# Optimization experiments

Measured on AMD Instinct MI355X. Metric: run time of the kernel, lower is better.

## Reference

```python
import jax, jax.numpy as jnp
import numpy as np

N_NODES = 10000
IN_FEATS = 50
HIDDEN = 512
OUT_FEATS = 121
N_EDGES = 160000


def setup_inputs() -> dict:
    key = jax.random.key(0)
    ks = jax.random.split(key, 8)
    x = jax.random.normal(ks[0], (N_NODES, IN_FEATS), dtype=jnp.float32)
    edge_index = jax.random.randint(ks[1], (2, N_EDGES), 0, N_NODES, dtype=jnp.int64)
    # SAGEConv params: lin_l applied to aggregated neighbors (carries bias), lin_r to self.
    def glorot(k, fan_in, fan_out):
        s = jnp.sqrt(6.0 / (fan_in + fan_out))
        return jax.random.uniform(k, (fan_in, fan_out), minval=-s, maxval=s, dtype=jnp.float32)
    W1_l = glorot(ks[2], IN_FEATS, HIDDEN)
    W1_r = glorot(ks[3], IN_FEATS, HIDDEN)
    b1 = jnp.zeros((HIDDEN,), dtype=jnp.float32)
    W2_l = glorot(ks[4], HIDDEN, OUT_FEATS)
    W2_r = glorot(ks[5], HIDDEN, OUT_FEATS)
    b2 = jnp.zeros((OUT_FEATS,), dtype=jnp.float32)
    return {"x": x, "edge_index": edge_index, "W1_l": W1_l, "W1_r": W1_r,
            "b1": b1, "W2_l": W2_l, "W2_r": W2_r, "b2": b2}


def _mean_agg(h, src, dst, n_nodes):
    # gather source features per edge, segment-sum at destination, divide by in-degree
    summed = jax.ops.segment_sum(h[src], dst, num_segments=n_nodes)  # [N, F]
    deg = jax.ops.segment_sum(jnp.ones((src.shape[0],), h.dtype), dst, num_segments=n_nodes)
    return summed / jnp.maximum(deg, 1.0)[:, None]


def _sage_conv(h, src, dst, W_l, W_r, b, n_nodes):
    agg = _mean_agg(h, src, dst, n_nodes)
    return agg @ W_l + h @ W_r + b


def reference(x, edge_index, W1_l, W1_r, b1, W2_l, W2_r, b2):
    src, dst = edge_index[0], edge_index[1]
    n = x.shape[0]
    h = _sage_conv(x, src, dst, W1_l, W1_r, b1, n)
    h = jax.nn.relu(h)
    # dropout is identity in eval mode
    out = _sage_conv(h, src, dst, W2_l, W2_r, b2, n)
    return out
```

## Files before the change

kernel.cpp:

```cpp
#include <hip/hip_runtime.h>
#include <hip/hip_bf16.h>

constexpr int NN   = 10000;
constexpr int INF  = 50;
constexpr int HID  = 512;
constexpr int OUTF = 121;
constexpr int NE   = 160000;
constexpr int DMAX = 64;

typedef __attribute__((ext_vector_type(8))) short short8;
typedef __attribute__((ext_vector_type(4))) float floatx4;

__device__ inline float bf2f(unsigned short u) {
    union { unsigned int i; float f; } v; v.i = ((unsigned)u) << 16; return v.f;
}
__device__ inline unsigned short f2bf(float f) {
    __hip_bfloat16 h = __float2bfloat16(f);
    return *(unsigned short*)&h;
}



__global__ __launch_bounds__(256) void k_fillprep(const int* __restrict__ srcv, const int* __restrict__ dstv,
                                                  unsigned* __restrict__ cursor, int* __restrict__ csr,
                                                  const float* __restrict__ x,
                                                  const float* __restrict__ W1l, const float* __restrict__ W1r,
                                                  const float* __restrict__ W2l, const float* __restrict__ W2r,
                                                  __hip_bfloat16* __restrict__ xp,
                                                  __hip_bfloat16* __restrict__ B1p, __hip_bfloat16* __restrict__ B2p) {
    int b = blockIdx.x;
    if (b < 625) {
        unsigned V = cursor[NN];
        int e = b * 256 + threadIdx.x;
        if (e < NE) {
            int d = dstv[e];
            if ((unsigned)d < (unsigned)NN) {
                int pos = (int)(atomicAdd(&cursor[d], 1u) - V);
                int s = min(max(srcv[e], 0), NN - 1);
                if ((unsigned)pos < (unsigned)DMAX) csr[d * DMAX + pos] = s;
            }
        }
    } else {
        int idx = (b - 625) * 256 + threadIdx.x;
        if (idx < 65536) {
            int j = idx & 7, L = (idx >> 3) & 63, kt = (idx >> 9) & 3, nt = idx >> 11;
            int k = kt * 32 + ((L >> 4) * 8 + j);
            int n = nt * 16 + (L & 15);
            float v = (k < 50) ? W1l[k * HID + n] : ((k < 100) ? W1r[(k - 50) * HID + n] : 0.f);
            B1p[idx] = __float2bfloat16(v);
        }
        {
            int j = idx & 7, L = (idx >> 3) & 63, kt = (idx >> 9) & 15, nt = idx >> 13;
            int k = kt * 32 + ((L >> 4) * 8 + j);
            int n = nt * 16 + (L & 15);
            float v;
            if (n < 128) v = (n < OUTF) ? W2l[k * OUTF + n] : 0.f;
            else { int c = n - 128; v = (c < OUTF) ? W2r[k * OUTF + c] : 0.f; }
            B2p[idx] = __float2bfloat16(v);
        }
        for (int r = idx; r < NN * 64; r += 131072) {
            int n = r >> 6, c = r & 63;
            xp[r] = __float2bfloat16(c < INF ? x[n * INF + c] : 0.f);
        }
    }
}


__global__ __launch_bounds__(1024, 4) void k_fused(const __hip_bfloat16* __restrict__ xp,
                                                   const unsigned* __restrict__ cursor, const int* __restrict__ csr,
                                                   const __hip_bfloat16* __restrict__ B1p,
                                                   const float* __restrict__ b1,
                                                   const __hip_bfloat16* __restrict__ B2p,
                                                   __hip_bfloat16* __restrict__ Pb,
                                                   __hip_bfloat16* __restrict__ Qb) {
    __shared__ __align__(16) unsigned short As[16 * 136];
    __shared__ __align__(16) unsigned short Ht[16 * 520];
    int t = threadIdx.x;
    int w = t >> 6, lane = t & 63, quad = lane >> 4, l16 = lane & 15;
    int m0 = blockIdx.x * 16;
    const unsigned short* xs = (const unsigned short*)xp;

    {
        int nu = __builtin_amdgcn_readfirstlane(m0 + w);
        unsigned V = cursor[NN];
        int dt = (int)(cursor[nu] - V);
        int d = min(dt, DMAX);
        const int* crow = csr + nu * DMAX;
        const unsigned* xw = (const unsigned*)xp;
        int half = lane >> 5;
        int cp = lane & 31;
        float lo0 = 0.f, hi0 = 0.f, lo1 = 0.f, hi1 = 0.f;
        float lo2 = 0.f, hi2 = 0.f, lo3 = 0.f, hi3 = 0.f;
        int j = 0;
        for (; j + 8 <= d; j += 8) {
            int a0 = crow[j],     b0 = crow[j + 1];
            int a1 = crow[j + 2], b1i = crow[j + 3];
            int a2 = crow[j + 4], b2i = crow[j + 5];
            int a3 = crow[j + 6], b3i = crow[j + 7];
            int r0 = half ? b0 : a0;
            int r1 = half ? b1i : a1;
            int r2 = half ? b2i : a2;
            int r3 = half ? b3i : a3;
            unsigned u0 = xw[r0 * 32 + cp];
            unsigned u1 = xw[r1 * 32 + cp];
            unsigned u2 = xw[r2 * 32 + cp];
            unsigned u3 = xw[r3 * 32 + cp];
            lo0 += __uint_as_float(u0 << 16); hi0 += __uint_as_float(u0 & 0xffff0000u);
            lo1 += __uint_as_float(u1 << 16); hi1 += __uint_as_float(u1 & 0xffff0000u);
            lo2 += __uint_as_float(u2 << 16); hi2 += __uint_as_float(u2 & 0xffff0000u);
            lo3 += __uint_as_float(u3 << 16); hi3 += __uint_as_float(u3 & 0xffff0000u);
        }
        for (; j + 2 <= d; j += 2) {
            int a = crow[j], b = crow[j + 1];
            int r = half ? b : a;
            unsigned u = xw[r * 32 + cp];
            lo0 += __uint_as_float(u << 16); hi0 += __uint_as_float(u & 0xffff0000u);
        }
        if (j < d && half == 0) {
            int a = crow[j];
            unsigned u = xw[a * 32 + cp];
            lo0 += __uint_as_float(u << 16); hi0 += __uint_as_float(u & 0xffff0000u);
        }
        float lo = (lo0 + lo1) + (lo2 + lo3);
        float hi = (hi0 + hi1) + (hi2 + hi3);
        lo += __shfl_xor(lo, 32);
        hi += __shfl_xor(hi, 32);
        float invd = (dt > 0) ? 1.f / (float)dt : 1.f;
        if (half == 0 && cp < 25) {
            unsigned pk = (unsigned)f2bf(lo * invd) | ((unsigned)f2bf(hi * invd) << 16);
            *(unsigned*)&As[w * 136 + 2 * cp] = pk;
        }
        As[w * 136 + 50 + lane] = xs[nu * 64 + lane];
        if (lane < 7) *(unsigned*)&As[w * 136 + 114 + 2 * lane] = 0u;
    }
    __syncthreads();

    short8 af[4];
#pragma unroll
    for (int ks = 0; ks < 4; ++ks) af[ks] = *(const short8*)&As[l16 * 136 + ks * 32 + quad * 8];
    {
        floatx4 acc[2];
#pragma unroll
        for (int nt = 0; nt < 2; ++nt) acc[nt] = floatx4{0.f, 0.f, 0.f, 0.f};
#pragma unroll
        for (int nt = 0; nt < 2; ++nt) {
            int ntile = w * 2 + nt;
            const short* Bb = (const short*)B1p + (ntile * 4 * 64 + lane) * 8;
#pragma unroll
            for (int ks = 0; ks < 4; ++ks) {
                short8 bf = *(const short8*)(Bb + ks * 512);
                acc[nt] = __builtin_amdgcn_mfma_f32_16x16x32_bf16(af[ks], bf, acc[nt], 0, 0, 0);
            }
        }
#pragma unroll
        for (int nt = 0; nt < 2; ++nt) {
            int col = w * 32 + nt * 16 + l16;
            float bias = b1[col];
#pragma unroll
            for (int r = 0; r < 4; ++r)
                Ht[(quad * 4 + r) * 520 + col] = f2bf(fmaxf(acc[nt][r] + bias, 0.f));
        }
    }
    __syncthreads();

    int isQ = w >> 3;
    int wh = w & 7;
    int ntile2 = isQ * 8 + wh;
    floatx4 acc = {0.f, 0.f, 0.f, 0.f};
    const short* Bc = (const short*)B2p + ((ntile2 * 16) * 64 + lane) * 8;
#pragma unroll 4
    for (int ks = 0; ks < 16; ++ks) {
        short8 a2 = *(const short8*)&Ht[l16 * 520 + ks * 32 + quad * 8];
        short8 bf = *(const short8*)(Bc + ks * 512);
        acc = __builtin_amdgcn_mfma_f32_16x16x32_bf16(a2, bf, acc, 0, 0, 0);
    }
    __hip_bfloat16* Out = isQ ? Qb : Pb;
#pragma unroll
    for (int r = 0; r < 4; ++r) {
        int row = m0 + quad * 4 + r;
        Out[row * 128 + wh * 16 + l16] = __float2bfloat16(acc[r]);
    }
}


__global__ __launch_bounds__(256) void k_final(const __hip_bfloat16* __restrict__ Pb,
                                               const __hip_bfloat16* __restrict__ Qb,
                                               const float* __restrict__ b2,
                                               const unsigned* __restrict__ cursor, const int* __restrict__ csr,
                                               float* __restrict__ out) {
    int lane = threadIdx.x & 63;
    int nu = __builtin_amdgcn_readfirstlane(blockIdx.x * 4 + (threadIdx.x >> 6));
    unsigned V = cursor[NN];
    int dt = (int)(cursor[nu] - V);
    int d = min(dt, DMAX);
    const int* crow = csr + nu * DMAX;
    const unsigned* Pw = (const unsigned*)Pb;
    const unsigned* Qw = (const unsigned*)Qb;
    float lo0 = 0.f, lo1 = 0.f, lo2 = 0.f, lo3 = 0.f;
    float hi0 = 0.f, hi1 = 0.f, hi2 = 0.f, hi3 = 0.f;
    int j = 0;
    for (; j + 8 <= d; j += 8) {
        int i0 = crow[j], i1 = crow[j + 1], i2 = crow[j + 2], i3 = crow[j + 3];
        int i4 = crow[j + 4], i5 = crow[j + 5], i6 = crow[j + 6], i7 = crow[j + 7];
        unsigned w0 = Pw[i0 * 64 + lane];
        unsigned w1 = Pw[i1 * 64 + lane];
        unsigned w2 = Pw[i2 * 64 + lane];
        unsigned w3 = Pw[i3 * 64 + lane];
        unsigned w4 = Pw[i4 * 64 + lane];
        unsigned w5 = Pw[i5 * 64 + lane];
        unsigned w6 = Pw[i6 * 64 + lane];
        unsigned w7 = Pw[i7 * 64 + lane];
        lo0 += __uint_as_float(w0 << 16); hi0 += __uint_as_float(w0 & 0xffff0000u);
        lo1 += __uint_as_float(w1 << 16); hi1 += __uint_as_float(w1 & 0xffff0000u);
        lo2 += __uint_as_float(w2 << 16); hi2 += __uint_as_float(w2 & 0xffff0000u);
        lo3 += __uint_as_float(w3 << 16); hi3 += __uint_as_float(w3 & 0xffff0000u);
        lo0 += __uint_as_float(w4 << 16); hi0 += __uint_as_float(w4 & 0xffff0000u);
        lo1 += __uint_as_float(w5 << 16); hi1 += __uint_as_float(w5 & 0xffff0000u);
        lo2 += __uint_as_float(w6 << 16); hi2 += __uint_as_float(w6 & 0xffff0000u);
        lo3 += __uint_as_float(w7 << 16); hi3 += __uint_as_float(w7 & 0xffff0000u);
    }
    for (; j < d; ++j) {
        int i0 = crow[j];
        unsigned w0 = Pw[i0 * 64 + lane];
        lo0 += __uint_as_float(w0 << 16); hi0 += __uint_as_float(w0 & 0xffff0000u);
    }
    float slo = (lo0 + lo1) + (lo2 + lo3);
    float shi = (hi0 + hi1) + (hi2 + hi3);
    float invd = (dt > 0) ? 1.f / (float)dt : 1.f;
    unsigned q = Qw[nu * 64 + lane];
    int c0 = lane * 2, c1 = lane * 2 + 1;
    if (c0 < OUTF) out[nu * OUTF + c0] = slo * invd + __uint_as_float(q << 16) + b2[c0];
    if (c1 < OUTF) out[nu * OUTF + c1] = shi * invd + __uint_as_float(q & 0xffff0000u) + b2[c1];
}

extern "C" void kernel_launch(void* const* d_in, const int* in_sizes, int n_in,
                              void* d_out, int out_size, void* d_ws, size_t ws_size,
                              hipStream_t stream) {
    const float* x   = (const float*)d_in[0];
    const int* edges = (const int*)d_in[1];
    const float* W1l = (const float*)d_in[2];
    const float* W1r = (const float*)d_in[3];
    const float* b1  = (const float*)d_in[4];
    const float* W2l = (const float*)d_in[5];
    const float* W2r = (const float*)d_in[6];
    const float* b2  = (const float*)d_in[7];
    float* out = (float*)d_out;

    char* ws = (char*)d_ws;
    unsigned* cursor    = (unsigned*)(ws + 0);
    int* csr            = (int*)(ws + 40064);
    __hip_bfloat16* xp  = (__hip_bfloat16*)(ws + 2600064);
    __hip_bfloat16* Pb  = (__hip_bfloat16*)(ws + 3880064);
    __hip_bfloat16* Qb  = (__hip_bfloat16*)(ws + 6440064);
    __hip_bfloat16* B1p = (__hip_bfloat16*)(ws + 9000064);
    __hip_bfloat16* B2p = (__hip_bfloat16*)(ws + 9131136);

    const int* srcv = edges;
    const int* dstv = edges + NE;

    k_fillprep<<<1137, 256, 0, stream>>>(srcv, dstv, cursor, csr,
                                         x, W1l, W1r, W2l, W2r, xp, B1p, B2p);
    k_fused<<<625, 1024, 0, stream>>>(xp, cursor, csr, B1p, b1, B2p, Pb, Qb);
    k_final<<<2500, 256, 0, stream>>>(Pb, Qb, b2, cursor, csr, out);
}
```

Measured before the change: 111.3 us.

## Merge three kernels into one cooperative persistent kernel with grid syncs

Replaces the three-kernel launch sequence (CSR fill/weight prep, fused two-layer GEMM, final aggregation) with a single cooperative kernel. The phases are separated by grid.sync() and each phase uses a grid-stride loop. Grid size comes from an occupancy query capped at 625 blocks. The aim is to remove the gaps between kernel launches. In exchange it adds grid-barrier cost and may run fewer concurrent blocks in the tile and final phases. The old launch path is kept as a fallback if the cooperative launch fails.

New measurement: 201.6 us. +81.1%, slower.

```diff
diff --git a/kernel.cpp b/kernel.cpp
--- a/kernel.cpp
+++ b/kernel.cpp
@@ -1,5 +1,8 @@
 #include <hip/hip_runtime.h>
 #include <hip/hip_bf16.h>
+#include <hip/hip_cooperative_groups.h>
+
+namespace cg = cooperative_groups;
 
 constexpr int NN   = 10000;
 constexpr int INF  = 50;
@@ -11,14 +14,221 @@
 typedef __attribute__((ext_vector_type(8))) short short8;
 typedef __attribute__((ext_vector_type(4))) float floatx4;
 
-__device__ inline float bf2f(unsigned short u) {
-    union { unsigned int i; float f; } v; v.i = ((unsigned)u) << 16; return v.f;
-}
 __device__ inline unsigned short f2bf(float f) {
     __hip_bfloat16 h = __float2bfloat16(f);
     return *(unsigned short*)&h;
 }
 
+
+
+__global__ __launch_bounds__(1024, 4) void k_mega(
+    const int* __restrict__ srcv, const int* __restrict__ dstv,
+    unsigned* __restrict__ cursor, int* __restrict__ csr,
+    const float* __restrict__ x,
+    const float* __restrict__ W1l, const float* __restrict__ W1r, const float* __restrict__ b1,
+    const float* __restrict__ W2l, const float* __restrict__ W2r, const float* __restrict__ b2,
+    __hip_bfloat16* __restrict__ xp, __hip_bfloat16* __restrict__ B1p, __hip_bfloat16* __restrict__ B2p,
+    __hip_bfloat16* __restrict__ Pb, __hip_bfloat16* __restrict__ Qb,
+    float* __restrict__ out)
+{
+    __shared__ __align__(16) unsigned short As[16 * 136];
+    __shared__ __align__(16) unsigned short Ht[16 * 520];
+    cg::grid_group grid = cg::this_grid();
+
+    const int t = threadIdx.x;
+    const int G = gridDim.x * 1024;
+    const int g0 = blockIdx.x * 1024 + t;
+
+    {
+        unsigned V = cursor[NN];
+        for (int e = g0; e < NE; e += G) {
+            int d = dstv[e];
+            if ((unsigned)d < (unsigned)NN) {
+                int pos = (int)(atomicAdd(&cursor[d], 1u) - V);
+                int s = min(max(srcv[e], 0), NN - 1);
+                if ((unsigned)pos < (unsigned)DMAX) csr[d * DMAX + pos] = s;
+            }
+        }
+        for (int idx = g0; idx < 65536; idx += G) {
+            int j = idx & 7, L = (idx >> 3) & 63, kt = (idx >> 9) & 3, nt = idx >> 11;
+            int k = kt * 32 + ((L >> 4) * 8 + j);
+            int n = nt * 16 + (L & 15);
+            float v = (k < 50) ? W1l[k * HID + n] : ((k < 100) ? W1r[(k - 50) * HID + n] : 0.f);
+            B1p[idx] = __float2bfloat16(v);
+        }
+        for (int idx = g0; idx < 131072; idx += G) {
+            int j = idx & 7, L = (idx >> 3) & 63, kt = (idx >> 9) & 15, nt = idx >> 13;
+            int k = kt * 32 + ((L >> 4) * 8 + j);
+            int n = nt * 16 + (L & 15);
+            float v;
+            if (n < 128) v = (n < OUTF) ? W2l[k * OUTF + n] : 0.f;
+            else { int c = n - 128; v = (c < OUTF) ? W2r[k * OUTF + c] : 0.f; }
+            B2p[idx] = __float2bfloat16(v);
+        }
+        for (int r = g0; r < NN * 64; r += G) {
+            int n = r >> 6, c = r & 63;
+            xp[r] = __float2bfloat16(c < INF ? x[n * INF + c] : 0.f);
+        }
+    }
+    grid.sync();
+
+    const int w = t >> 6, lane = t & 63, quad = lane >> 4, l16 = lane & 15;
+    const unsigned short* xs = (const unsigned short*)xp;
+    const unsigned Vs = cursor[NN];
+
+    for (int tile = blockIdx.x; tile < 625; tile += gridDim.x) {
+        int m0 = tile * 16;
+        {
+            int nu = __builtin_amdgcn_readfirstlane(m0 + w);
+            int dt = (int)(cursor[nu] - Vs);
+            int d = min(dt, DMAX);
+            const int* crow = csr + nu * DMAX;
+            const unsigned* xw = (const unsigned*)xp;
+            int half = lane >> 5;
+            int cp = lane & 31;
+            float lo0 = 0.f, hi0 = 0.f, lo1 = 0.f, hi1 = 0.f;
+            float lo2 = 0.f, hi2 = 0.f, lo3 = 0.f, hi3 = 0.f;
+            int j = 0;
+            for (; j + 8 <= d; j += 8) {
+                int a0 = crow[j],     b0 = crow[j + 1];
+                int a1 = crow[j + 2], b1i = crow[j + 3];
+                int a2 = crow[j + 4], b2i = crow[j + 5];
+                int a3 = crow[j + 6], b3i = crow[j + 7];
+                int r0 = half ? b0 : a0;
+                int r1 = half ? b1i : a1;
+                int r2 = half ? b2i : a2;
+                int r3 = half ? b3i : a3;
+                unsigned u0 = xw[r0 * 32 + cp];
+                unsigned u1 = xw[r1 * 32 + cp];
+                unsigned u2 = xw[r2 * 32 + cp];
+                unsigned u3 = xw[r3 * 32 + cp];
+                lo0 += __uint_as_float(u0 << 16); hi0 += __uint_as_float(u0 & 0xffff0000u);
+                lo1 += __uint_as_float(u1 << 16); hi1 += __uint_as_float(u1 & 0xffff0000u);
+                lo2 += __uint_as_float(u2 << 16); hi2 += __uint_as_float(u2 & 0xffff0000u);
+                lo3 += __uint_as_float(u3 << 16); hi3 += __uint_as_float(u3 & 0xffff0000u);
+            }
+            for (; j + 2 <= d; j += 2) {
+                int a = crow[j], b = crow[j + 1];
+                int r = half ? b : a;
+                unsigned u = xw[r * 32 + cp];
+                lo0 += __uint_as_float(u << 16); hi0 += __uint_as_float(u & 0xffff0000u);
+            }
+            if (j < d && half == 0) {
+                int a = crow[j];
+                unsigned u = xw[a * 32 + cp];
+                lo0 += __uint_as_float(u << 16); hi0 += __uint_as_float(u & 0xffff0000u);
+            }
+            float lo = (lo0 + lo1) + (lo2 + lo3);
+            float hi = (hi0 + hi1) + (hi2 + hi3);
+            lo += __shfl_xor(lo, 32);
+            hi += __shfl_xor(hi, 32);
+            float invd = (dt > 0) ? 1.f / (float)dt : 1.f;
+            if (half == 0 && cp < 25) {
+                unsigned pk = (unsigned)f2bf(lo * invd) | ((unsigned)f2bf(hi * invd) << 16);
+                *(unsigned*)&As[w * 136 + 2 * cp] = pk;
+            }
+            As[w * 136 + 50 + lane] = xs[nu * 64 + lane];
+            if (lane < 7) *(unsigned*)&As[w * 136 + 114 + 2 * lane] = 0u;
+        }
+        __syncthreads();
+
+        {
+            short8 af[4];
+#pragma unroll
+            for (int ks = 0; ks < 4; ++ks) af[ks] = *(const short8*)&As[l16 * 136 + ks * 32 + quad * 8];
+            floatx4 acc[2];
+#pragma unroll
+            for (int nt = 0; nt < 2; ++nt) acc[nt] = floatx4{0.f, 0.f, 0.f, 0.f};
+#pragma unroll
+            for (int nt = 0; nt < 2; ++nt) {
+                int ntile = w * 2 + nt;
+                const short* Bb = (const short*)B1p + (ntile * 4 * 64 + lane) * 8;
+#pragma unroll
+                for (int ks = 0; ks < 4; ++ks) {
+                    short8 bf = *(const short8*)(Bb + ks * 512);
+                    acc[nt] = __builtin_amdgcn_mfma_f32_16x16x32_bf16(af[ks], bf, acc[nt], 0, 0, 0);
+                }
+            }
+#pragma unroll
+            for (int nt = 0; nt < 2; ++nt) {
+                int col = w * 32 + nt * 16 + l16;
+                float bias = b1[col];
+#pragma unroll
+                for (int r = 0; r < 4; ++r)
+                    Ht[(quad * 4 + r) * 520 + col] = f2bf(fmaxf(acc[nt][r] + bias, 0.f));
+            }
+        }
+        __syncthreads();
+
+        {
+            int isQ = w >> 3;
+            int wh = w & 7;
+            int ntile2 = isQ * 8 + wh;
+            floatx4 acc = {0.f, 0.f, 0.f, 0.f};
+            const short* Bc = (const short*)B2p + ((ntile2 * 16) * 64 + lane) * 8;
+#pragma unroll 4
+            for (int ks = 0; ks < 16; ++ks) {
+                short8 a2 = *(const short8*)&Ht[l16 * 520 + ks * 32 + quad * 8];
+                short8 bf = *(const short8*)(Bc + ks * 512);
+                acc = __builtin_amdgcn_mfma_f32_16x16x32_bf16(a2, bf, acc, 0, 0, 0);
+            }
+            __hip_bfloat16* Op = isQ ? Qb : Pb;
+#pragma unroll
+            for (int r = 0; r < 4; ++r) {
+                int row = m0 + quad * 4 + r;
+                Op[row * 128 + wh * 16 + l16] = __float2bfloat16(acc[r]);
+            }
+        }
+    }
+    grid.sync();
+
+    {
+        const int totalWaves = gridDim.x * 16;
+        for (int nu_ = blockIdx.x * 16 + w; nu_ < NN; nu_ += totalWaves) {
+            int nu = __builtin_amdgcn_readfirstlane(nu_);
+            int dt = (int)(cursor[nu] - Vs);
+            int d = min(dt, DMAX);
+            const int* crow = csr + nu * DMAX;
+            const unsigned* Pw = (const unsigned*)Pb;
+            const unsigned* Qw = (const unsigned*)Qb;
+            float lo0 = 0.f, lo1 = 0.f, lo2 = 0.f, lo3 = 0.f;
+            float hi0 = 0.f, hi1 = 0.f, hi2 = 0.f, hi3 = 0.f;
+            int j = 0;
+            for (; j + 8 <= d; j += 8) {
+                int i0 = crow[j], i1 = crow[j + 1], i2 = crow[j + 2], i3 = crow[j + 3];
+                int i4 = crow[j + 4], i5 = crow[j + 5], i6 = crow[j + 6], i7 = crow[j + 7];
+                unsigned w0 = Pw[i0 * 64 + lane];
+                unsigned w1 = Pw[i1 * 64 + lane];
+                unsigned w2 = Pw[i2 * 64 + lane];
+                unsigned w3 = Pw[i3 * 64 + lane];
+                unsigned w4 = Pw[i4 * 64 + lane];
+                unsigned w5 = Pw[i5 * 64 + lane];
+                unsigned w6 = Pw[i6 * 64 + lane];
+                unsigned w7 = Pw[i7 * 64 + lane];
+                lo0 += __uint_as_float(w0 << 16); hi0 += __uint_as_float(w0 & 0xffff0000u);
+                lo1 += __uint_as_float(w1 << 16); hi1 += __uint_as_float(w1 & 0xffff0000u);
+                lo2 += __uint_as_float(w2 << 16); hi2 += __uint_as_float(w2 & 0xffff0000u);
+                lo3 += __uint_as_float(w3 << 16); hi3 += __uint_as_float(w3 & 0xffff0000u);
+                lo0 += __uint_as_float(w4 << 16); hi0 += __uint_as_float(w4 & 0xffff0000u);
+                lo1 += __uint_as_float(w5 << 16); hi1 += __uint_as_float(w5 & 0xffff0000u);
+                lo2 += __uint_as_float(w6 << 16); hi2 += __uint_as_float(w6 & 0xffff0000u);
+                lo3 += __uint_as_float(w7 << 16); hi3 += __uint_as_float(w7 & 0xffff0000u);
+            }
+            for (; j < d; ++j) {
+                int i0 = crow[j];
+                unsigned w0 = Pw[i0 * 64 + lane];
+                lo0 += __uint_as_float(w0 << 16); hi0 += __uint_as_float(w0 & 0xffff0000u);
+            }
+            float slo = (lo0 + lo1) + (lo2 + lo3);
+            float shi = (hi0 + hi1) + (hi2 + hi3);
+            float invd = (dt > 0) ? 1.f / (float)dt : 1.f;
+            unsigned q = Qw[nu * 64 + lane];
+            int c0 = lane * 2, c1 = lane * 2 + 1;
+            if (c0 < OUTF) out[nu * OUTF + c0] = slo * invd + __uint_as_float(q << 16) + b2[c0];
+            if (c1 < OUTF) out[nu * OUTF + c1] = shi * invd + __uint_as_float(q & 0xffff0000u) + b2[c1];
+        }
+    }
+}
 
 
 __global__ __launch_bounds__(256) void k_fillprep(const int* __restrict__ srcv, const int* __restrict__ dstv,
@@ -65,7 +275,6 @@
     }
 }
 
-
 __global__ __launch_bounds__(1024, 4) void k_fused(const __hip_bfloat16* __restrict__ xp,
                                                    const unsigned* __restrict__ cursor, const int* __restrict__ csr,
                                                    const __hip_bfloat16* __restrict__ B1p,
@@ -79,7 +288,6 @@
     int w = t >> 6, lane = t & 63, quad = lane >> 4, l16 = lane & 15;
     int m0 = blockIdx.x * 16;
     const unsigned short* xs = (const unsigned short*)xp;
-
     {
         int nu = __builtin_amdgcn_readfirstlane(m0 + w);
         unsigned V = cursor[NN];
@@ -134,7 +342,6 @@
         if (lane < 7) *(unsigned*)&As[w * 136 + 114 + 2 * lane] = 0u;
     }
     __syncthreads();
-
     short8 af[4];
 #pragma unroll
     for (int ks = 0; ks < 4; ++ks) af[ks] = *(const short8*)&As[l16 * 136 + ks * 32 + quad * 8];
@@ -162,7 +369,6 @@
         }
     }
     __syncthreads();
-
     int isQ = w >> 3;
     int wh = w & 7;
     int ntile2 = isQ * 8 + wh;
@@ -174,14 +380,13 @@
         short8 bf = *(const short8*)(Bc + ks * 512);
         acc = __builtin_amdgcn_mfma_f32_16x16x32_bf16(a2, bf, acc, 0, 0, 0);
     }
-    __hip_bfloat16* Out = isQ ? Qb : Pb;
+    __hip_bfloat16* Op = isQ ? Qb : Pb;
 #pragma unroll
     for (int r = 0; r < 4; ++r) {
         int row = m0 + quad * 4 + r;
-        Out[row * 128 + wh * 16 + l16] = __float2bfloat16(acc[r]);
-    }
-}
-
+        Op[row * 128 + wh * 16 + l16] = __float2bfloat16(acc[r]);
+    }
+}
 
 __global__ __launch_bounds__(256) void k_final(const __hip_bfloat16* __restrict__ Pb,
                                                const __hip_bfloat16* __restrict__ Qb,
@@ -258,8 +463,28 @@
     const int* srcv = edges;
     const int* dstv = edges + NE;
 
-    k_fillprep<<<1137, 256, 0, stream>>>(srcv, dstv, cursor, csr,
-                                         x, W1l, W1r, W2l, W2r, xp, B1p, B2p);
-    k_fused<<<625, 1024, 0, stream>>>(xp, cursor, csr, B1p, b1, B2p, Pb, Qb);
-    k_final<<<2500, 256, 0, stream>>>(Pb, Qb, b2, cursor, csr, out);
-}
+    static int nblk = 0;
+    if (nblk == 0) {
+        int maxb = 0;
+        hipError_t qe = hipOccupancyMaxActiveBlocksPerMultiprocessor(
+            &maxb, reinterpret_cast<const void*>(&k_mega), 1024, 0);
+        if (qe != hipSuccess || maxb < 1) maxb = 1;
+        nblk = 256 * maxb;
+        if (nblk > 625) nblk = 625;
+    }
+
+    void* args[] = { (void*)&srcv, (void*)&dstv, (void*)&cursor, (void*)&csr,
+                     (void*)&x, (void*)&W1l, (void*)&W1r, (void*)&b1,
+                     (void*)&W2l, (void*)&W2r, (void*)&b2,
+                     (void*)&xp, (void*)&B1p, (void*)&B2p,
+                     (void*)&Pb, (void*)&Qb, (void*)&out };
+    hipError_t err = hipLaunchCooperativeKernel(
+        reinterpret_cast<void*>(&k_mega), dim3(nblk), dim3(1024), args, 0, stream);
+
+    if (err != hipSuccess) {
+        k_fillprep<<<1137, 256, 0, stream>>>(srcv, dstv, cursor, csr,
+                                             x, W1l, W1r, W2l, W2r, xp, B1p, B2p);
+        k_fused<<<625, 1024, 0, stream>>>(xp, cursor, csr, B1p, b1, B2p, Pb, Qb);
+        k_final<<<2500, 256, 0, stream>>>(Pb, Qb, b2, cursor, csr, out);
+    }
+}
```
